# Kernel tuning notes

Measured on AMD Instinct MI355X. Metric: run time of the kernel, lower is better.

Reference implementation:

```python
import jax, jax.numpy as jnp
import numpy as np

B, C, H, W = 2, 64, 270, 480
CQ = C // 8


def _distance_weight(n):
    i = jnp.arange(n, dtype=jnp.float32)
    d = i[None, :] - i[:, None]  # j - i
    return jnp.exp(-(d * d) / (2.0 * (n * n / 4.0)))  # [n, n]


def setup_inputs() -> dict:
    key = jax.random.key(0)
    ks = jax.random.split(key, 8)
    s = 0.05
    return {
        "x": jax.random.normal(ks[0], (B, C, H, W), jnp.float32),
        "Wq": jax.random.normal(ks[1], (CQ, C), jnp.float32) * s,
        "bq": jax.random.normal(ks[2], (CQ,), jnp.float32) * s,
        "Wk": jax.random.normal(ks[3], (CQ, C), jnp.float32) * s,
        "bk": jax.random.normal(ks[4], (CQ,), jnp.float32) * s,
        "Wv": jax.random.normal(ks[5], (C, C), jnp.float32) * s,
        "bv": jax.random.normal(ks[6], (C,), jnp.float32) * s,
        "gamma": jax.random.normal(ks[7], (), jnp.float32) * 0.3,
        "dw_h": _distance_weight(H),  # [H, H] non-trainable buffer
        "dw_w": _distance_weight(W),  # [W, W] non-trainable buffer
    }


def reference(x, Wq, bq, Wk, bk, Wv, bv, gamma, dw_h, dw_w):
    # 1x1 convs == per-pixel linear projections
    q = jnp.einsum('oc,bchw->bohw', Wq, x) + bq[None, :, None, None]  # [B,CQ,H,W]
    k = jnp.einsum('oc,bchw->bohw', Wk, x) + bk[None, :, None, None]  # [B,CQ,H,W]
    v = jnp.einsum('oc,bchw->bohw', Wv, x) + bv[None, :, None, None]  # [B,C,H,W]

    height, width = x.shape[2], x.shape[3]
    neg_inf = jnp.float32(-jnp.inf)

    # row (H-direction) energy: queries/keys along the height axis per column w
    e_h = jnp.einsum('bchw,bcgw->bwhg', q, k) * dw_h[None, None]  # [B,W,H,H]
    # diagonal -inf mask (dw_h diag == 1, so order of mul is immaterial)
    eye_h = jnp.eye(height, dtype=bool)
    e_h = jnp.where(eye_h[None, None], neg_inf, e_h)
    e_h = jnp.transpose(e_h, (0, 2, 1, 3))  # [B,H,W,H]

    # column (W-direction) energy along the width axis per row h
    e_w = jnp.einsum('bchw,bchv->bhwv', q, k) * dw_w[None, None]  # [B,H,W,W]

    # joint softmax over concatenated H and W directions
    att = jax.nn.softmax(jnp.concatenate([e_h, e_w], axis=3), axis=3)  # [B,H,W,H+W]
    att_h = jnp.transpose(att[:, :, :, :height], (0, 2, 1, 3))  # [B,W,H,H]
    att_w = att[:, :, :, height:]  # [B,H,W,W]

    out_h = jnp.einsum('bcgw,bwhg->bchw', v, att_h)  # [B,C,H,W]
    out_w = jnp.einsum('bchv,bhwv->bchw', v, att_w)  # [B,C,H,W]

    return gamma * (out_h + out_w) + x
```

## Files before the change

kernel.cpp:

```cpp
#include <hip/hip_runtime.h>
#include <hip/hip_bf16.h>

namespace {

constexpr int B  = 2;
constexpr int C  = 64;
constexpr int CQ = 8;
constexpr int H  = 270;
constexpr int W  = 480;
constexpr int HW = H * W;
constexpr float INVH2 = 2.0f / (270.0f * 270.0f);
constexpr float INVW2 = 2.0f / (480.0f * 480.0f);

typedef __attribute__((ext_vector_type(4))) float f32x4;
typedef __attribute__((ext_vector_type(8))) short short8;
typedef __attribute__((ext_vector_type(4))) unsigned int uint4v;

__device__ __forceinline__ float bits2f(unsigned short u) {
  union { unsigned int i; float f; } cv;
  cv.i = ((unsigned int)u) << 16;
  return cv.f;
}

__device__ __forceinline__ unsigned short f2bf(float f) {
  union { __hip_bfloat16 b; unsigned short u; } cv;
  cv.b = __float2bfloat16(f);
  return cv.u;
}

__device__ __forceinline__ unsigned int pack2(float a, float b) {
  return ((unsigned int)f2bf(b) << 16) | (unsigned int)f2bf(a);
}

__device__ __forceinline__ short8 pack_p(const float p0[4], const float p1[4]) {
  uint4v pw;
  pw[0] = pack2(p0[0], p0[1]);
  pw[1] = pack2(p0[2], p0[3]);
  pw[2] = pack2(p1[0], p1[1]);
  pw[3] = pack2(p1[2], p1[3]);
  return __builtin_bit_cast(short8, pw);
}


__global__ __launch_bounds__(256)
void k_qkv(const float* __restrict__ x,
           const float* __restrict__ Wq, const float* __restrict__ bq,
           const float* __restrict__ Wk, const float* __restrict__ bk,
           const float* __restrict__ Wv, const float* __restrict__ bv,
           unsigned short* __restrict__ qwp, unsigned short* __restrict__ kwp,
           unsigned short* __restrict__ qhp, unsigned short* __restrict__ khp,
           unsigned short* __restrict__ v, unsigned short* __restrict__ vt) {
  __shared__ __align__(16) float wql[CQ * C];
  __shared__ __align__(16) float wkl[CQ * C];
  __shared__ __align__(16) float wvl[C * C];
  __shared__ float bql[CQ], bkl[CQ], bvl[C];
  const int tid = threadIdx.x;
  for (int i = tid; i < CQ * C; i += 256) { wql[i] = Wq[i]; wkl[i] = Wk[i]; }
  for (int i = tid; i < C * C; i += 256) wvl[i] = Wv[i];
  if (tid < CQ) { bql[tid] = bq[tid]; bkl[tid] = bk[tid]; }
  if (tid < C) bvl[tid] = bv[tid];
  __syncthreads();
  const int pix = blockIdx.x * 256 + tid;
  if (pix >= B * HW) return;
  const int b = pix / HW;
  const int r = pix - b * HW;
  const int h = r / W;
  const int w = r - h * W;

  float qa[CQ], ka[CQ], va[C];
#pragma unroll
  for (int o = 0; o < CQ; ++o) { qa[o] = bql[o]; ka[o] = bkl[o]; }
#pragma unroll
  for (int o = 0; o < C; ++o) va[o] = bvl[o];

  const float* xp = x + (size_t)b * C * HW + r;
  for (int c = 0; c < C; c += 4) {
    const float x0 = xp[(size_t)(c + 0) * HW];
    const float x1 = xp[(size_t)(c + 1) * HW];
    const float x2 = xp[(size_t)(c + 2) * HW];
    const float x3 = xp[(size_t)(c + 3) * HW];
#pragma unroll
    for (int o = 0; o < CQ; ++o) {
      const float4 a = *(const float4*)(wql + o * C + c);
      qa[o] = fmaf(a.w, x3, fmaf(a.z, x2, fmaf(a.y, x1, fmaf(a.x, x0, qa[o]))));
      const float4 bb = *(const float4*)(wkl + o * C + c);
      ka[o] = fmaf(bb.w, x3, fmaf(bb.z, x2, fmaf(bb.y, x1, fmaf(bb.x, x0, ka[o]))));
    }
#pragma unroll
    for (int o = 0; o < C; ++o) {
      const float4 cc = *(const float4*)(wvl + o * C + c);
      va[o] = fmaf(cc.w, x3, fmaf(cc.z, x2, fmaf(cc.y, x1, fmaf(cc.x, x0, va[o]))));
    }
  }

  uint4 qp4, kp4;
  qp4.x = pack2(qa[0], qa[1]); qp4.y = pack2(qa[2], qa[3]);
  qp4.z = pack2(qa[4], qa[5]); qp4.w = pack2(qa[6], qa[7]);
  kp4.x = pack2(ka[0], ka[1]); kp4.y = pack2(ka[2], ka[3]);
  kp4.z = pack2(ka[4], ka[5]); kp4.w = pack2(ka[6], ka[7]);
  *(uint4*)(qwp + (size_t)pix * 8) = qp4;
  *(uint4*)(kwp + (size_t)pix * 8) = kp4;
  const size_t tbase = ((size_t)b * W + w) * H + h;
  *(uint4*)(qhp + tbase * 8) = qp4;
  *(uint4*)(khp + tbase * 8) = kp4;

  unsigned short* vp = v + (size_t)b * C * HW + r;
#pragma unroll
  for (int o = 0; o < C; ++o) vp[(size_t)o * HW] = f2bf(va[o]);
  unsigned short* vtp = vt + tbase * C;
#pragma unroll
  for (int j = 0; j < 16; ++j) {
    ushort4 u;
    u.x = f2bf(va[4 * j + 0]);
    u.y = f2bf(va[4 * j + 1]);
    u.z = f2bf(va[4 * j + 2]);
    u.w = f2bf(va[4 * j + 3]);
    *(ushort4*)(vtp + 4 * j) = u;
  }
}

constexpr int VSW = 494;

__global__ __launch_bounds__(512, 1)
void k_outw(const unsigned short* __restrict__ qwp,
            const unsigned short* __restrict__ kwp,
            const unsigned short* __restrict__ v,
            unsigned short* __restrict__ ow, float* __restrict__ Sw) {
  __shared__ __align__(16) unsigned short vbs[64 * VSW];
  __shared__ __align__(16) unsigned short kls[480 * 8];
  const int h = blockIdx.x >> 1, z = blockIdx.x & 1;
  const int b = blockIdx.y;
  const int tid = threadIdx.x;
  const size_t rowbase = ((size_t)b * H + h) * W;

  const unsigned short* vrow = v + (size_t)b * C * HW + (size_t)h * W;
  ushort4 vr0[8];
#pragma unroll
  for (int it = 0; it < 8; ++it) {
    const int idx = tid + it * 512;
    const int c = idx / 120, s4 = (idx - c * 120) * 4;
    vr0[it] = *(const ushort4*)(vrow + (size_t)c * HW + s4);
  }
  uint4 kreg;
  if (tid < 480) kreg = *(const uint4*)(kwp + (rowbase + tid) * 8);
#pragma unroll
  for (int it = 0; it < 8; ++it) {
    const int idx = tid + it * 512;
    const int c = idx / 120, s4 = (idx - c * 120) * 4;
    const int u = s4 & 31;
    const int t = (u < 16) ? ((u >> 2) * 8) : (((u - 16) >> 2) * 8 + 4);
    *(ushort4*)(vbs + c * VSW + (s4 & ~31) + t) = vr0[it];
  }
  ushort4 vr1[7];
#pragma unroll
  for (int it = 0; it < 7; ++it) {
    const int idx = tid + (8 + it) * 512;
    const int c = idx / 120, s4 = (idx - c * 120) * 4;
    vr1[it] = *(const ushort4*)(vrow + (size_t)c * HW + s4);
  }
#pragma unroll
  for (int it = 0; it < 7; ++it) {
    const int idx = tid + (8 + it) * 512;
    const int c = idx / 120, s4 = (idx - c * 120) * 4;
    const int u = s4 & 31;
    const int t = (u < 16) ? ((u >> 2) * 8) : (((u - 16) >> 2) * 8 + 4);
    *(ushort4*)(vbs + c * VSW + (s4 & ~31) + t) = vr1[it];
  }
  if (tid < 480) *(uint4*)(kls + tid * 8) = kreg;

  const int lane = tid & 63, wv = tid >> 6;
  const int l15 = lane & 15, quad = lane >> 4;
  const int chunk = z * 8 + wv;
  const bool active = chunk < 15;
  const int m0 = chunk * 32;

  short8 qa0 = short8{0, 0, 0, 0, 0, 0, 0, 0};
  short8 qa1 = short8{0, 0, 0, 0, 0, 0, 0, 0};
  if (quad == 0 && active) {
    qa0 = *(const short8*)(qwp + (rowbase + m0 + l15) * 8);
    qa1 = *(const short8*)(qwp + (rowbase + m0 + 16 + l15) * 8);
  }

  f32x4 acc[2][4];
  float Sacc[2] = {0.0f, 0.0f};
#pragma unroll
  for (int mt = 0; mt < 2; ++mt)
#pragma unroll
    for (int ct = 0; ct < 4; ++ct)
#pragma unroll
      for (int rr = 0; rr < 4; ++rr) acc[mt][ct][rr] = 0.0f;

  __syncthreads();

  if (active) {
    short8 kb0 = short8{0, 0, 0, 0, 0, 0, 0, 0};
    short8 kb1 = short8{0, 0, 0, 0, 0, 0, 0, 0};
    if (quad == 0) {
      kb0 = *(const short8*)(kls + (l15) * 8);
      kb1 = *(const short8*)(kls + (16 + l15) * 8);
    }
    for (int ci = 0; ci < 15; ++ci) {
      const int sc = ci * 32;
      short8 nk0 = short8{0, 0, 0, 0, 0, 0, 0, 0};
      short8 nk1 = short8{0, 0, 0, 0, 0, 0, 0, 0};
      if (ci < 14 && quad == 0) {
        nk0 = *(const short8*)(kls + (sc + 32 + l15) * 8);
        nk1 = *(const short8*)(kls + (sc + 48 + l15) * 8);
      }
      short8 vb[4];
#pragma unroll
      for (int ct = 0; ct < 4; ++ct)
        vb[ct] = *(const short8*)(vbs + (ct * 16 + l15) * VSW + sc + quad * 8);
      const f32x4 z4 = f32x4{0.f, 0.f, 0.f, 0.f};
      const f32x4 E00 = __builtin_amdgcn_mfma_f32_16x16x32_bf16(kb0, qa0, z4, 0, 0, 0);
      const f32x4 E01 = __builtin_amdgcn_mfma_f32_16x16x32_bf16(kb1, qa0, z4, 0, 0, 0);
      const f32x4 E10 = __builtin_amdgcn_mfma_f32_16x16x32_bf16(kb0, qa1, z4, 0, 0, 0);
      const f32x4 E11 = __builtin_amdgcn_mfma_f32_16x16x32_bf16(kb1, qa1, z4, 0, 0, 0);
#pragma unroll
      for (int mt = 0; mt < 2; ++mt) {
        const int m = m0 + mt * 16 + l15;
        const f32x4 Ea = mt ? E10 : E00;
        const f32x4 Eb = mt ? E11 : E01;
        float p0[4], p1[4];
#pragma unroll
        for (int rr = 0; rr < 4; ++rr) {
          const float d0 = (float)(m - (sc + quad * 4 + rr));
          const float d1 = d0 - 16.0f;
          p0[rr] = __expf(Ea[rr] * __expf(-(d0 * d0) * INVW2));
          p1[rr] = __expf(Eb[rr] * __expf(-(d1 * d1) * INVW2));
          Sacc[mt] += p0[rr] + p1[rr];
        }
        const short8 pa = pack_p(p0, p1);
#pragma unroll
        for (int ct = 0; ct < 4; ++ct)
          acc[mt][ct] = __builtin_amdgcn_mfma_f32_16x16x32_bf16(pa, vb[ct], acc[mt][ct], 0, 0, 0);
      }
      kb0 = nk0;
      kb1 = nk1;
    }

#pragma unroll
    for (int mt = 0; mt < 2; ++mt) {
      float s = Sacc[mt];
      s += __shfl_xor(s, 16);
      s += __shfl_xor(s, 32);
      if (lane < 16) Sw[rowbase + m0 + mt * 16 + l15] = s;
    }
  }

  __syncthreads();
  unsigned short* ob = vbs;
  if (active) {
#pragma unroll
    for (int mt = 0; mt < 2; ++mt)
#pragma unroll
      for (int ct = 0; ct < 4; ++ct)
#pragma unroll
        for (int rr = 0; rr < 4; ++rr)
          ob[(ct * 16 + l15) * VSW + m0 + mt * 16 + quad * 4 + rr] = f2bf(acc[mt][ct][rr]);
  }
  __syncthreads();
  unsigned short* og = ow + ((size_t)b * H + h) * C * W;
  const int mlo = z ? 256 : 0;
  const int nu = z ? 112 : 128;
  for (int idx = tid; idx < 64 * nu; idx += 512) {
    const int c = idx / nu, i = idx - c * nu;
    *(unsigned int*)(og + (size_t)c * W + mlo + 2 * i) =
        *(const unsigned int*)(ob + c * VSW + mlo + 2 * i);
  }
}

constexpr int VSH = 302;

__global__ __launch_bounds__(576, 1)
void k_outh(const unsigned short* __restrict__ qhp,
            const unsigned short* __restrict__ khp,
            const unsigned short* __restrict__ vt,
            unsigned short* __restrict__ oht, float* __restrict__ Sht) {
  __shared__ __align__(16) unsigned short vbs[64 * VSH];
  __shared__ __align__(16) unsigned short kls[288 * 8];
  const int w = blockIdx.x;
  const int b = blockIdx.y;
  const int tid = threadIdx.x;
  const size_t colbase = ((size_t)b * W + w) * H;

  const unsigned short* vtb = vt + colbase * C;
  ushort4 vreg[8];
#pragma unroll
  for (int it = 0; it < 8; ++it) {
    const int idx = tid + it * 576;
    const int g = idx >> 4, c4 = (idx & 15) * 4;
    vreg[it] = (g < H) ? *(const ushort4*)(vtb + (size_t)g * C + c4)
                       : make_ushort4(0, 0, 0, 0);
  }
  uint4 kreg;
  if (tid < 288) kreg = *(const uint4*)(khp + (colbase + min(tid, H - 1)) * 8);
#pragma unroll
  for (int it = 0; it < 8; ++it) {
    const int idx = tid + it * 576;
    const int g = idx >> 4, c4 = (idx & 15) * 4;
    const int u = g & 31;
    const int t = (u < 16) ? ((u >> 2) * 8 + (u & 3))
                           : (((u - 16) >> 2) * 8 + 4 + (u & 3));
    const int slot = (g & ~31) + t;
    vbs[(c4 + 0) * VSH + slot] = vreg[it].x;
    vbs[(c4 + 1) * VSH + slot] = vreg[it].y;
    vbs[(c4 + 2) * VSH + slot] = vreg[it].z;
    vbs[(c4 + 3) * VSH + slot] = vreg[it].w;
  }
  if (tid < 288) *(uint4*)(kls + tid * 8) = kreg;

  const int lane = tid & 63, wv = tid >> 6;
  const int l15 = lane & 15, quad = lane >> 4;
  const int m0 = wv * 32;

  short8 qa0 = short8{0, 0, 0, 0, 0, 0, 0, 0};
  short8 qa1 = short8{0, 0, 0, 0, 0, 0, 0, 0};
  if (quad == 0) {
    qa0 = *(const short8*)(qhp + (colbase + min(m0 + l15, H - 1)) * 8);
    qa1 = *(const short8*)(qhp + (colbase + min(m0 + 16 + l15, H - 1)) * 8);
  }

  f32x4 acc[2][4];
  float Sacc[2] = {0.0f, 0.0f};
#pragma unroll
  for (int mt = 0; mt < 2; ++mt)
#pragma unroll
    for (int ct = 0; ct < 4; ++ct)
#pragma unroll
      for (int rr = 0; rr < 4; ++rr) acc[mt][ct][rr] = 0.0f;

  __syncthreads();

  {
    short8 kb0 = short8{0, 0, 0, 0, 0, 0, 0, 0};
    short8 kb1 = short8{0, 0, 0, 0, 0, 0, 0, 0};
    if (quad == 0) {
      kb0 = *(const short8*)(kls + (l15) * 8);
      kb1 = *(const short8*)(kls + (16 + l15) * 8);
    }
    for (int ci = 0; ci < 9; ++ci) {
      const int gc = ci * 32;
      short8 nk0 = short8{0, 0, 0, 0, 0, 0, 0, 0};
      short8 nk1 = short8{0, 0, 0, 0, 0, 0, 0, 0};
      if (ci < 8 && quad == 0) {
        nk0 = *(const short8*)(kls + (gc + 32 + l15) * 8);
        nk1 = *(const short8*)(kls + (gc + 48 + l15) * 8);
      }
      short8 vb[4];
#pragma unroll
      for (int ct = 0; ct < 4; ++ct)
        vb[ct] = *(const short8*)(vbs + (ct * 16 + l15) * VSH + gc + quad * 8);
      const f32x4 z4 = f32x4{0.f, 0.f, 0.f, 0.f};
      const f32x4 E00 = __builtin_amdgcn_mfma_f32_16x16x32_bf16(kb0, qa0, z4, 0, 0, 0);
      const f32x4 E01 = __builtin_amdgcn_mfma_f32_16x16x32_bf16(kb1, qa0, z4, 0, 0, 0);
      const f32x4 E10 = __builtin_amdgcn_mfma_f32_16x16x32_bf16(kb0, qa1, z4, 0, 0, 0);
      const f32x4 E11 = __builtin_amdgcn_mfma_f32_16x16x32_bf16(kb1, qa1, z4, 0, 0, 0);
#pragma unroll
      for (int mt = 0; mt < 2; ++mt) {
        const int m = m0 + mt * 16 + l15;
        const f32x4 Ea = mt ? E10 : E00;
        const f32x4 Eb = mt ? E11 : E01;
        float p0[4], p1[4];
#pragma unroll
        for (int rr = 0; rr < 4; ++rr) {
          const int g0 = gc + quad * 4 + rr;
          const int g1 = g0 + 16;
          const float d0 = (float)(m - g0);
          const float d1 = d0 - 16.0f;
          p0[rr] = (g0 < H && g0 != m)
                       ? __expf(Ea[rr] * __expf(-(d0 * d0) * INVH2)) : 0.0f;
          p1[rr] = (g1 < H && g1 != m)
                       ? __expf(Eb[rr] * __expf(-(d1 * d1) * INVH2)) : 0.0f;
          Sacc[mt] += p0[rr] + p1[rr];
        }
        const short8 pa = pack_p(p0, p1);
#pragma unroll
        for (int ct = 0; ct < 4; ++ct)
          acc[mt][ct] = __builtin_amdgcn_mfma_f32_16x16x32_bf16(pa, vb[ct], acc[mt][ct], 0, 0, 0);
      }
      kb0 = nk0;
      kb1 = nk1;
    }
  }

#pragma unroll
  for (int mt = 0; mt < 2; ++mt) {
    float s = Sacc[mt];
    s += __shfl_xor(s, 16);
    s += __shfl_xor(s, 32);
    const int m = m0 + mt * 16 + l15;
    if (lane < 16 && m < H) Sht[colbase + m] = s;
  }

  __syncthreads();
  unsigned short* ob = vbs;
#pragma unroll
  for (int mt = 0; mt < 2; ++mt)
#pragma unroll
    for (int ct = 0; ct < 4; ++ct)
#pragma unroll
      for (int rr = 0; rr < 4; ++rr)
        ob[(ct * 16 + l15) * VSH + m0 + mt * 16 + quad * 4 + rr] = f2bf(acc[mt][ct][rr]);
  __syncthreads();
  unsigned short* og = oht + ((size_t)b * W + w) * C * H;
  for (int idx = tid; idx < 64 * 135; idx += 576) {
    const int c = idx / 135, hp = idx - c * 135;
    *(unsigned int*)(og + (size_t)c * H + 2 * hp) =
        *(const unsigned int*)(ob + c * VSH + 2 * hp);
  }
}

__global__ __launch_bounds__(256)
void k_combine(const unsigned short* __restrict__ oht,
               const unsigned short* __restrict__ ow,
               const float* __restrict__ Sht, const float* __restrict__ Sw,
               const float* __restrict__ x,
               const float* __restrict__ gp,
               float* __restrict__ out) {
  __shared__ float tile[32][33];
  const int b = blockIdx.z >> 6, c = blockIdx.z & 63;
  const int w0 = blockIdx.x * 32, h0 = blockIdx.y * 32;
  const int tx = threadIdx.x, ty = threadIdx.y;
#pragma unroll
  for (int i = 0; i < 4; ++i) {
    const int wl = ty + i * 8;
    const int hh = h0 + tx;
    float val = 0.0f;
    if (hh < H) val = bits2f(oht[(((size_t)b * W + (w0 + wl)) * C + c) * H + hh]);
    tile[wl][tx] = val;
  }
  __syncthreads();
  const float gamma = *gp;
#pragma unroll
  for (int i = 0; i < 4; ++i) {
    const int hl = ty + i * 8;
    const int hh = h0 + hl;
    if (hh < H) {
      const int ww = w0 + tx;
      const float uh = tile[tx][hl];
      const float uw = bits2f(ow[(((size_t)b * H + hh) * C + c) * W + ww]);
      const size_t si = ((size_t)b * H + hh) * W + ww;
      const float Z = Sht[((size_t)b * W + ww) * H + hh] + Sw[si];
      const float invZ = __builtin_amdgcn_rcpf(Z);
      const size_t xi = ((size_t)b * C + c) * HW + (size_t)hh * W + ww;
      out[xi] = fmaf(gamma * invZ, uh + uw, x[xi]);
    }
  }
}

}

extern "C" void kernel_launch(void* const* d_in, const int* in_sizes, int n_in,
                              void* d_out, int out_size, void* d_ws, size_t ws_size,
                              hipStream_t stream) {
  (void)in_sizes; (void)n_in; (void)out_size; (void)ws_size;
  const float* x  = (const float*)d_in[0];
  const float* Wq = (const float*)d_in[1];
  const float* bq = (const float*)d_in[2];
  const float* Wk = (const float*)d_in[3];
  const float* bk = (const float*)d_in[4];
  const float* Wv = (const float*)d_in[5];
  const float* bv = (const float*)d_in[6];
  const float* gp = (const float*)d_in[7];
  float* out = (float*)d_out;

  char* p = (char*)d_ws;
  auto take = [&](size_t bytes) -> void* {
    char* r = p;
    p += (bytes + 255) & ~(size_t)255;
    return (void*)r;
  };
  unsigned short* qwp = (unsigned short*)take(sizeof(unsigned short) * (size_t)B * HW * 8);
  unsigned short* kwp = (unsigned short*)take(sizeof(unsigned short) * (size_t)B * HW * 8);
  unsigned short* qhp = (unsigned short*)take(sizeof(unsigned short) * (size_t)B * HW * 8);
  unsigned short* khp = (unsigned short*)take(sizeof(unsigned short) * (size_t)B * HW * 8);
  unsigned short* v   = (unsigned short*)take(sizeof(unsigned short) * (size_t)B * C * HW);
  unsigned short* vt  = (unsigned short*)take(sizeof(unsigned short) * (size_t)B * C * HW);
  unsigned short* oht = (unsigned short*)take(sizeof(unsigned short) * (size_t)B * C * HW);
  unsigned short* owb = (unsigned short*)take(sizeof(unsigned short) * (size_t)B * C * HW);
  float* Sht = (float*)take(sizeof(float) * (size_t)B * HW);
  float* Sw  = (float*)take(sizeof(float) * (size_t)B * HW);

  hipLaunchKernelGGL(k_qkv, dim3((B * HW + 255) / 256), dim3(256), 0, stream,
                     x, Wq, bq, Wk, bk, Wv, bv, qwp, kwp, qhp, khp, v, vt);
  hipLaunchKernelGGL(k_outh, dim3(W, B), dim3(576), 0, stream,
                     qhp, khp, vt, oht, Sht);
  hipLaunchKernelGGL(k_outw, dim3(2 * H, B), dim3(512), 0, stream,
                     qwp, kwp, v, owb, Sw);
  hipLaunchKernelGGL(k_combine, dim3(W / 32, (H + 31) / 32, B * C), dim3(32, 8), 0, stream,
                     oht, owb, Sht, Sw, x, gp, out);
}
```

Measured before the change: 433.9 us.

## Split each column of k_outh across two blocks of 16-row query tiles

The H-direction attention kernel now launches two blocks per column, each handling half of the query rows with one 16-row tile per wave instead of two. This doubles the block count (960 per batch) to improve occupancy and load balance across CUs and lowers per-thread register pressure. In exchange, each column's V and K data is loaded into shared memory twice, and the K-fragment prefetch across iterations was dropped.

```diff
diff --git a/kernel.cpp b/kernel.cpp
--- a/kernel.cpp
+++ b/kernel.cpp
@@ -279,7 +279,7 @@
             unsigned short* __restrict__ oht, float* __restrict__ Sht) {
   __shared__ __align__(16) unsigned short vbs[64 * VSH];
   __shared__ __align__(16) unsigned short kls[288 * 8];
-  const int w = blockIdx.x;
+  const int w = blockIdx.x >> 1, z = blockIdx.x & 1;
   const int b = blockIdx.y;
   const int tid = threadIdx.x;
   const size_t colbase = ((size_t)b * W + w) * H;
@@ -312,102 +312,78 @@
 
   const int lane = tid & 63, wv = tid >> 6;
   const int l15 = lane & 15, quad = lane >> 4;
-  const int m0 = wv * 32;
-
-  short8 qa0 = short8{0, 0, 0, 0, 0, 0, 0, 0};
-  short8 qa1 = short8{0, 0, 0, 0, 0, 0, 0, 0};
-  if (quad == 0) {
-    qa0 = *(const short8*)(qhp + (colbase + min(m0 + l15, H - 1)) * 8);
-    qa1 = *(const short8*)(qhp + (colbase + min(m0 + 16 + l15, H - 1)) * 8);
-  }
-
-  f32x4 acc[2][4];
-  float Sacc[2] = {0.0f, 0.0f};
-#pragma unroll
-  for (int mt = 0; mt < 2; ++mt)
-#pragma unroll
-    for (int ct = 0; ct < 4; ++ct)
-#pragma unroll
-      for (int rr = 0; rr < 4; ++rr) acc[mt][ct][rr] = 0.0f;
-
-  __syncthreads();
-
-  {
+  const int m0 = (z * 9 + wv) * 16;
+  const int m = m0 + l15;
+
+  short8 qa = short8{0, 0, 0, 0, 0, 0, 0, 0};
+  if (quad == 0)
+    qa = *(const short8*)(qhp + (colbase + min(m, H - 1)) * 8);
+
+  f32x4 acc[4];
+  float Sacc = 0.0f;
+#pragma unroll
+  for (int ct = 0; ct < 4; ++ct)
+#pragma unroll
+    for (int rr = 0; rr < 4; ++rr) acc[ct][rr] = 0.0f;
+
+  __syncthreads();
+
+  for (int ci = 0; ci < 9; ++ci) {
+    const int gc = ci * 32;
     short8 kb0 = short8{0, 0, 0, 0, 0, 0, 0, 0};
     short8 kb1 = short8{0, 0, 0, 0, 0, 0, 0, 0};
     if (quad == 0) {
-      kb0 = *(const short8*)(kls + (l15) * 8);
-      kb1 = *(const short8*)(kls + (16 + l15) * 8);
-    }
-    for (int ci = 0; ci < 9; ++ci) {
-      const int gc = ci * 32;
-      short8 nk0 = short8{0, 0, 0, 0, 0, 0, 0, 0};
-      short8 nk1 = short8{0, 0, 0, 0, 0, 0, 0, 0};
-      if (ci < 8 && quad == 0) {
-        nk0 = *(const short8*)(kls + (gc + 32 + l15) * 8);
-        nk1 = *(const short8*)(kls + (gc + 48 + l15) * 8);
-      }
-      short8 vb[4];
-#pragma unroll
-      for (int ct = 0; ct < 4; ++ct)
-        vb[ct] = *(const short8*)(vbs + (ct * 16 + l15) * VSH + gc + quad * 8);
-      const f32x4 z4 = f32x4{0.f, 0.f, 0.f, 0.f};
-      const f32x4 E00 = __builtin_amdgcn_mfma_f32_16x16x32_bf16(kb0, qa0, z4, 0, 0, 0);
-      const f32x4 E01 = __builtin_amdgcn_mfma_f32_16x16x32_bf16(kb1, qa0, z4, 0, 0, 0);
-      const f32x4 E10 = __builtin_amdgcn_mfma_f32_16x16x32_bf16(kb0, qa1, z4, 0, 0, 0);
-      const f32x4 E11 = __builtin_amdgcn_mfma_f32_16x16x32_bf16(kb1, qa1, z4, 0, 0, 0);
-#pragma unroll
-      for (int mt = 0; mt < 2; ++mt) {
-        const int m = m0 + mt * 16 + l15;
-        const f32x4 Ea = mt ? E10 : E00;
-        const f32x4 Eb = mt ? E11 : E01;
-        float p0[4], p1[4];
-#pragma unroll
-        for (int rr = 0; rr < 4; ++rr) {
-          const int g0 = gc + quad * 4 + rr;
-          const int g1 = g0 + 16;
-          const float d0 = (float)(m - g0);
-          const float d1 = d0 - 16.0f;
-          p0[rr] = (g0 < H && g0 != m)
-                       ? __expf(Ea[rr] * __expf(-(d0 * d0) * INVH2)) : 0.0f;
-          p1[rr] = (g1 < H && g1 != m)
-                       ? __expf(Eb[rr] * __expf(-(d1 * d1) * INVH2)) : 0.0f;
-          Sacc[mt] += p0[rr] + p1[rr];
-        }
-        const short8 pa = pack_p(p0, p1);
-#pragma unroll
-        for (int ct = 0; ct < 4; ++ct)
-          acc[mt][ct] = __builtin_amdgcn_mfma_f32_16x16x32_bf16(pa, vb[ct], acc[mt][ct], 0, 0, 0);
-      }
-      kb0 = nk0;
-      kb1 = nk1;
-    }
-  }
-
-#pragma unroll
-  for (int mt = 0; mt < 2; ++mt) {
-    float s = Sacc[mt];
+      kb0 = *(const short8*)(kls + (gc + l15) * 8);
+      kb1 = *(const short8*)(kls + (gc + 16 + l15) * 8);
+    }
+    short8 vb[4];
+#pragma unroll
+    for (int ct = 0; ct < 4; ++ct)
+      vb[ct] = *(const short8*)(vbs + (ct * 16 + l15) * VSH + gc + quad * 8);
+    const f32x4 z4 = f32x4{0.f, 0.f, 0.f, 0.f};
+    const f32x4 E0 = __builtin_amdgcn_mfma_f32_16x16x32_bf16(kb0, qa, z4, 0, 0, 0);
+    const f32x4 E1 = __builtin_amdgcn_mfma_f32_16x16x32_bf16(kb1, qa, z4, 0, 0, 0);
+    float p0[4], p1[4];
+#pragma unroll
+    for (int rr = 0; rr < 4; ++rr) {
+      const int g0 = gc + quad * 4 + rr;
+      const int g1 = g0 + 16;
+      const float d0 = (float)(m - g0);
+      const float d1 = d0 - 16.0f;
+      p0[rr] = (g0 < H && g0 != m)
+                   ? __expf(E0[rr] * __expf(-(d0 * d0) * INVH2)) : 0.0f;
+      p1[rr] = (g1 < H && g1 != m)
+                   ? __expf(E1[rr] * __expf(-(d1 * d1) * INVH2)) : 0.0f;
+      Sacc += p0[rr] + p1[rr];
+    }
+    const short8 pa = pack_p(p0, p1);
+#pragma unroll
+    for (int ct = 0; ct < 4; ++ct)
+      acc[ct] = __builtin_amdgcn_mfma_f32_16x16x32_bf16(pa, vb[ct], acc[ct], 0, 0, 0);
+  }
+
+  {
+    float s = Sacc;
     s += __shfl_xor(s, 16);
     s += __shfl_xor(s, 32);
-    const int m = m0 + mt * 16 + l15;
     if (lane < 16 && m < H) Sht[colbase + m] = s;
   }
 
   __syncthreads();
   unsigned short* ob = vbs;
 #pragma unroll
-  for (int mt = 0; mt < 2; ++mt)
-#pragma unroll
-    for (int ct = 0; ct < 4; ++ct)
-#pragma unroll
-      for (int rr = 0; rr < 4; ++rr)
-        ob[(ct * 16 + l15) * VSH + m0 + mt * 16 + quad * 4 + rr] = f2bf(acc[mt][ct][rr]);
+  for (int ct = 0; ct < 4; ++ct)
+#pragma unroll
+    for (int rr = 0; rr < 4; ++rr)
+      ob[(ct * 16 + l15) * VSH + m0 + quad * 4 + rr] = f2bf(acc[ct][rr]);
   __syncthreads();
   unsigned short* og = oht + ((size_t)b * W + w) * C * H;
-  for (int idx = tid; idx < 64 * 135; idx += 576) {
-    const int c = idx / 135, hp = idx - c * 135;
-    *(unsigned int*)(og + (size_t)c * H + 2 * hp) =
-        *(const unsigned int*)(ob + c * VSH + 2 * hp);
+  const int mlo = z ? 144 : 0;
+  const int nu = z ? 63 : 72;
+  for (int idx = tid; idx < 64 * nu; idx += 576) {
+    const int c = idx / nu, i = idx - c * nu;
+    *(unsigned int*)(og + (size_t)c * H + mlo + 2 * i) =
+        *(const unsigned int*)(ob + c * VSH + mlo + 2 * i);
   }
 }
 
@@ -484,7 +460,7 @@
 
   hipLaunchKernelGGL(k_qkv, dim3((B * HW + 255) / 256), dim3(256), 0, stream,
                      x, Wq, bq, Wk, bk, Wv, bv, qwp, kwp, qhp, khp, v, vt);
-  hipLaunchKernelGGL(k_outh, dim3(W, B), dim3(576), 0, stream,
+  hipLaunchKernelGGL(k_outh, dim3(2 * W, B), dim3(576), 0, stream,
                      qhp, khp, vt, oht, Sht);
   hipLaunchKernelGGL(k_outw, dim3(2 * H, B), dim3(512), 0, stream,
                      qwp, kwp, v, owb, Sw);
```

New measurement: 405.0 us. 6.7% less time.
